# Kernel optimization log

Hardware: AMD Instinct MI355X
Metric: run time of the kernel (lower is better)

## Reference

```python
import jax, jax.numpy as jnp
import numpy as np
from jax import lax

SHIFT = 32  # shift_range from init
EPS_NORM = 1e-12
EPS_MASK = 1e-6


def _l2_normalize_flat(x):
    # F.normalize(x.reshape(B,-1)): per-sample L2 normalize with eps 1e-12
    B = x.shape[0]
    flat = x.reshape(B, -1)
    n = jnp.linalg.norm(flat, axis=1, keepdims=True)
    return (flat / jnp.maximum(n, EPS_NORM)).reshape(x.shape)


def setup_inputs() -> dict:
    key = jax.random.key(0)
    k1, k2 = jax.random.split(key)
    grd_feature = jax.random.normal(k1, (8, 32, 32, 32), dtype=jnp.float32)
    sat_feature = jax.random.normal(k2, (8, 32, 128, 128), dtype=jnp.float32)
    return {"grd_feature": grd_feature, "sat_feature": sat_feature, "test_method": 1}


def reference(grd_feature, sat_feature, test_method):
    # test_method == 1 path (default); test_method in {0,1} only differ in divisor
    M, C, H_s, W_s = sat_feature.shape
    N, _, H, W = grd_feature.shape
    kH = min(H, H_s - 2 * SHIFT)
    kW = min(W, W_s - 2 * SHIFT)

    # center-crop ground template to (kH, kW) and L2-normalize per sample
    gh0, gw0 = H // 2 - kH // 2, W // 2 - kW // 2
    grd = grd_feature[:, :, gh0:gh0 + 2 * (kH // 2), gw0:gw0 + 2 * (kW // 2)]
    N_, _, H_k, W_k = grd.shape
    grd = _l2_normalize_flat(grd)

    # center-crop satellite to search region and L2-normalize per sample
    sh0 = H_s // 2 - SHIFT - kH // 2
    sw0 = W_s // 2 - SHIFT - kW // 2
    sat = sat_feature[:, :, sh0:sh0 + 2 * (SHIFT + kH // 2), sw0:sw0 + 2 * (SHIFT + kW // 2)]
    _, _, H_i, W_i = sat.shape
    sat = _l2_normalize_flat(sat)

    # all-pairs cross-correlation: corr[m, n, y, x] (torch grouped-conv on repeated sat
    # is equivalent to a plain VALID conv of sat with all N ground filters)
    corr = lax.conv_general_dilated(
        sat, grd, window_strides=(1, 1), padding='VALID',
        dimension_numbers=('NCHW', 'OIHW', 'NCHW'))  # [M, N, Ho, Wo]
    Ho, Wo = corr.shape[2], corr.shape[3]

    # sliding-window sum of |sat|^2 (avg_pool with divisor_override=1, summed over C)
    s2 = jnp.sum(sat * sat, axis=1)  # [M, H_i, W_i]
    partical = lax.reduce_window(s2, jnp.float32(0), lax.add,
                                 (1, H_k, W_k), (1, 1, 1), 'VALID')  # [M, Ho, Wo]
    if test_method == 0:
        denom = jnp.sqrt(partical)
    else:
        denom = partical
    corr = corr / jnp.maximum(denom[:, None], EPS_NORM)

    similarity_matrix = jnp.max(corr, axis=(2, 3))  # [M, N]

    # diagonal pairs (m == n): peak localization
    diag = jnp.diagonal(corr, axis1=0, axis2=1)        # [Ho, Wo, M]
    diag = jnp.transpose(diag, (2, 0, 1)).reshape(M, -1)
    max_index = jnp.argmax(diag, axis=-1)
    pos_h = max_index // Wo
    pos_w = max_index % Wo

    grd_mask = (jnp.abs(jnp.sum(grd, axis=1)) > EPS_MASK).astype(jnp.float32)  # [N, H_k, W_k]

    def place(ph, pw, gm):
        z = jnp.zeros((1, H_i, W_i), dtype=jnp.float32)
        return lax.dynamic_update_slice(z, gm[None], (0, ph, pw))

    mask = jax.vmap(place)(pos_h, pos_w, grd_mask)  # [M, 1, H_i, W_i]
    return similarity_matrix, mask
```

## Files before the change

kernel.cpp:

```cpp
#include <hip/hip_runtime.h>
#include <stdint.h>

typedef unsigned short u16;
typedef unsigned int u32;
typedef unsigned long long u64;
typedef __bf16 bf16x8 __attribute__((ext_vector_type(8)));
typedef float floatx4 __attribute__((ext_vector_type(4)));

#define DEVI static __device__ __forceinline__

DEVI u16 f2bf(float f) {
  uint32_t u = __builtin_bit_cast(uint32_t, f);
  u += 0x7FFFu + ((u >> 16) & 1u);
  return (u16)(u >> 16);
}
DEVI float bf2f(u16 b) { return __builtin_bit_cast(float, (uint32_t)b << 16); }

DEVI u32 encf(float f) {
  u32 u = __builtin_bit_cast(u32, f);
  return (u >> 31) ? ~u : (u | 0x80000000u);
}
DEVI float decf(u32 e) {
  u32 u = (e >> 31) ? (e & 0x7FFFFFFFu) : ~e;
  return __builtin_bit_cast(float, u);
}

DEVI void cp16(const u16* g, u16* l) {
#if __has_builtin(__builtin_amdgcn_global_load_lds)
  __builtin_amdgcn_global_load_lds(
      (const __attribute__((address_space(1))) uint32_t*)g,
      (__attribute__((address_space(3))) uint32_t*)l, 16, 0, 0);
#else
  *(uint4*)l = *(const uint4*)g;
#endif
}

static constexpr size_t OFF_CORRP = 0;
static constexpr size_t OFF_SATT  = OFF_CORRP + (size_t)4*270400*4;
static constexpr size_t OFF_GRDP  = OFF_SATT + (size_t)8*4*96*96*8*2;
static constexpr size_t OFF_S2    = OFF_GRDP + (size_t)4*1024*16*8*2;
static constexpr size_t OFF_PART  = OFF_S2   + (size_t)73728*4;
static constexpr size_t OFF_NRMP  = OFF_PART + (size_t)33800*4;
static constexpr size_t OFF_GNRM  = OFF_NRMP + 768*4;
static constexpr size_t OFF_MASK  = OFF_GNRM + 32;
static constexpr size_t OFF_PMAX  = OFF_MASK + (size_t)8192*4;
static constexpr size_t OFF_CNT   = OFF_PMAX + 320*4;
static constexpr size_t OFF_CAND  = OFF_CNT  + 512;

__global__ __launch_bounds__(256) void k_prep(
    const float* __restrict__ grd, const float* __restrict__ sat,
    u16* __restrict__ sTh, u16* __restrict__ gP,
    float* __restrict__ s2, float* __restrict__ nrmp,
    float* __restrict__ gnrm, float* __restrict__ gmask,
    u32* __restrict__ cnts) {
  __shared__ float L[32*100];
  __shared__ float red[256];
  const int t = threadIdx.x;
  if (blockIdx.x < 768) {
    const int m = blockIdx.x / 96, y = blockIdx.x - (blockIdx.x / 96) * 96;
    #pragma unroll
    for (int k = 0; k < 3; ++k) {
      const int idx = k*256 + t;
      const int c = idx / 24, xq = idx - c*24;
      const float4 v = *(const float4*)(sat + (((size_t)m*32 + c)*128 + (16+y))*128 + 16 + xq*4);
      *(float4*)(&L[c*100 + xq*4]) = v;
    }
    __syncthreads();
    float ss = 0.f;
    if (t < 96) {
      #pragma unroll
      for (int c = 0; c < 32; ++c) { const float v = L[c*100 + t]; ss += v*v; }
      s2[(size_t)m*9216 + y*96 + t] = ss;
    }
    red[t] = ss; __syncthreads();
    for (int s = 128; s > 0; s >>= 1) { if (t < s) red[t] += red[t+s]; __syncthreads(); }
    if (t == 0) nrmp[m*96 + y] = red[0];
    for (int idx = t; idx < 384; idx += 256) {
      const int cb = idx / 96, x = idx - cb*96;
      union { u16 us[8]; uint4 v4; } P;
      #pragma unroll
      for (int e = 0; e < 8; ++e) P.us[e] = f2bf(L[(cb*8+e)*100 + x]);
      *(uint4*)(&sTh[(((size_t)m*4+cb)*9216 + (size_t)y*96 + x)*8]) = P.v4;
    }
  } else if (blockIdx.x == 776) {
    if (t < 72) cnts[t] = 0u;
  } else {
    const int n = blockIdx.x - 768;
    float nn = 0.f, scs[4];
    #pragma unroll
    for (int it = 0; it < 4; ++it) {
      const int pidx = it*256 + t;
      float vals[32]; float sc = 0.f;
      #pragma unroll
      for (int c = 0; c < 32; ++c) {
        const float v = grd[((size_t)n*32 + c)*1024 + pidx];
        vals[c] = v; sc += v; nn += v*v;
      }
      scs[it] = sc;
      #pragma unroll
      for (int cb = 0; cb < 4; ++cb) {
        union { u16 us[8]; uint4 v4; } ph, pl;
        #pragma unroll
        for (int e = 0; e < 8; ++e) {
          const float v = vals[cb*8+e];
          const u16 h = f2bf(v); ph.us[e] = h; pl.us[e] = f2bf(v - bf2f(h));
        }
        const size_t o = ((size_t)cb*1024 + pidx)*128;
        *(uint4*)(&gP[o + (size_t)n*8])     = ph.v4;
        *(uint4*)(&gP[o + (size_t)(n+8)*8]) = pl.v4;
      }
    }
    red[t] = nn; __syncthreads();
    for (int s = 128; s > 0; s >>= 1) { if (t < s) red[t] += red[t+s]; __syncthreads(); }
    const float gn = fmaxf(sqrtf(red[0]), 1e-12f);
    if (t == 0) gnrm[n] = red[0];
    const float thr = 1e-6f * gn;
    #pragma unroll
    for (int it = 0; it < 4; ++it)
      gmask[n*1024 + it*256 + t] = (fabsf(scs[it]) > thr) ? 1.f : 0.f;
  }
}

__global__ __launch_bounds__(256, 3) void k_conv(
    const u16* __restrict__ satT, const u16* __restrict__ gP,
    const float* __restrict__ s2, float* __restrict__ corr_p,
    float* __restrict__ part)
{
  __shared__ __align__(16) u16 patch[41*48*8];

  const int bi = blockIdx.x;
  const int tid = threadIdx.x;

  if (bi < 72) {
    float* S  = (float*)patch;
    float* HS = S + 40*96;
    const int pm = bi / 9, ysl = (bi - pm*9)*8;
    const int nrows = (65 - ysl) < 8 ? (65 - ysl) : 8;
    const int scnt  = (96 - ysl) < 40 ? (96 - ysl) : 40;
    for (int idx = tid; idx < scnt*96; idx += 256)
      S[idx] = s2[(size_t)pm*9216 + (size_t)ysl*96 + idx];
    __syncthreads();
    const int hrows = nrows + 31;
    for (int idx = tid; idx < hrows*65; idx += 256) {
      const int r = idx / 65, xo = idx - r*65;
      const float* p = &S[r*96 + xo];
      float s = 0.f;
      #pragma unroll
      for (int j = 0; j < 32; ++j) s += p[j];
      HS[idx] = s;
    }
    __syncthreads();
    for (int idx = tid; idx < nrows*65; idx += 256) {
      const int r = idx / 65, xo = idx - r*65;
      float s = 0.f;
      #pragma unroll
      for (int i = 0; i < 32; ++i) s += HS[(r+i)*65 + xo];
      part[(size_t)pm*4225 + (size_t)(ysl+r)*65 + xo] = s;
    }
    return;
  }

  const int wave = tid >> 6, lane = tid & 63;
  const int pr = lane & 15, q = lane >> 4;

  if (bi >= 968) {
    const int e = bi - 968;
    const int cb = e & 3;
    const int yt = (e >> 2) % 5;
    const int m  = e / 20;
    const int ybase = yt * 13;
    const size_t rowbase = ((size_t)(m*4 + cb) * 96 + ybase) * 96;
    for (int k = tid; k < 44*32; k += 256) {
      const int rho = k >> 5, px = k & 31;
      cp16(&satT[(rowbase + (size_t)rho*96 + 64 + px)*8], &patch[(size_t)k*8]);
    }
    asm volatile("s_waitcnt vmcnt(0)" ::: "memory");
    __syncthreads();
    const int prc = pr < 13 ? pr : 12;
    floatx4 acc = (floatx4){0.f, 0.f, 0.f, 0.f};
    #pragma unroll
    for (int jbi = 0; jbi < 2; ++jbi) {
      const int jb = wave*2 + jbi;
      const int px_e = jb*4 + q;
      const u16* bp = gP + ((size_t)cb*1024 + (size_t)(jb*4+q))*128 + (size_t)pr*8;
      uint4 Br[8];
      #pragma unroll
      for (int ii = 0; ii < 8; ++ii) Br[ii] = *(const uint4*)(bp + (size_t)ii*4096);
      uint4 Ah[8];
      #pragma unroll
      for (int s = 0; s < 6; ++s)
        Ah[s] = *(const uint4*)(&patch[((size_t)(prc + s)*32 + px_e)*8]);
      #pragma unroll
      for (int i = 0; i < 32; ++i) {
        if (i < 26)
          Ah[(i+6)&7] = *(const uint4*)(&patch[((size_t)(prc + i + 6)*32 + px_e)*8]);
        const bf16x8 bf = __builtin_bit_cast(bf16x8, Br[i&7]);
        if (i < 24)
          Br[(i+8)&7] = *(const uint4*)(bp + (size_t)(i+8)*4096);
        acc = __builtin_amdgcn_mfma_f32_16x16x32_bf16(
            __builtin_bit_cast(bf16x8, Ah[i&7]), bf, acc, 0, 0, 0);
      }
    }
    float v4[4];
    #pragma unroll
    for (int k = 0; k < 4; ++k) v4[k] = acc[k] + __shfl_xor(acc[k], 8);
    __syncthreads();
    float* red = (float*)patch;
    #pragma unroll
    for (int k = 0; k < 4; ++k) red[((size_t)wave*64 + lane)*5 + k] = v4[k];
    __syncthreads();
    if (wave == 0 && pr < 8) {
      #pragma unroll
      for (int k = 0; k < 4; ++k) {
        const int yoff = q*4 + k;
        if (yoff < 13) {
          float s = 0.f;
          #pragma unroll
          for (int w = 0; w < 4; ++w) s += red[((size_t)w*64 + lane)*5 + k];
          corr_p[(size_t)cb*270400 + ((size_t)(m*8+pr)*65 + (ybase+yoff))*65 + 64] = s;
        }
      }
    }
    return;
  }

  int b = bi - 72;
  const int cb = b & 3; b >>= 2;
  const int xt = b & 3; b >>= 2;
  const int yt = b % 7;
  const int m  = b / 7;
  const int x0 = xt*16;

  if (yt < 6) {
    const int y0 = yt*10;
    const size_t rowbase = ((size_t)(m*4 + cb) * 96 + y0) * 96;
    for (int k = tid; k < 41*48; k += 256) {
      const int rho = k / 48, px = k - (k/48)*48;
      cp16(&satT[(rowbase + (size_t)rho*96 + x0 + px)*8], &patch[(size_t)k*8]);
    }
    asm volatile("s_waitcnt vmcnt(0)" ::: "memory");
    __syncthreads();

    floatx4 acc[10];
    #pragma unroll
    for (int r = 0; r < 10; ++r) acc[r] = (floatx4){0.f, 0.f, 0.f, 0.f};

    #pragma unroll
    for (int jbi = 0; jbi < 2; ++jbi) {
      const int jb = wave*2 + jbi;
      const int apx = pr + jb*4 + q;
      const u16* bp = gP + ((size_t)cb*1024 + (size_t)(jb*4+q))*128 + (size_t)pr*8;

      uint4 Br[8];
      #pragma unroll
      for (int ii = 0; ii < 8; ++ii) Br[ii] = *(const uint4*)(bp + (size_t)ii*4096);
      uint4 Ah[12];
      #pragma unroll
      for (int s = 0; s < 12; ++s) Ah[s] = *(const uint4*)(&patch[((size_t)s*48 + apx)*8]);

      #pragma unroll
      for (int i = 0; i < 32; ++i) {
        const bf16x8 bf = __builtin_bit_cast(bf16x8, Br[i&7]);
        if (i < 24)
          Br[(i+8)&7] = *(const uint4*)(bp + (size_t)(i+8)*4096);
        #pragma unroll
        for (int r = 0; r < 10; ++r)
          acc[r] = __builtin_amdgcn_mfma_f32_16x16x32_bf16(
              __builtin_bit_cast(bf16x8, Ah[(i+r)%12]), bf, acc[r], 0, 0, 0);
        if (i < 29)
          Ah[(i+12)%12] = *(const uint4*)(&patch[((size_t)(i+12)*48 + apx)*8]);
      }
    }

    float vals[40];
    #pragma unroll
    for (int r = 0; r < 10; ++r)
      #pragma unroll
      for (int k = 0; k < 4; ++k)
        vals[r*4+k] = acc[r][k] + __shfl_xor(acc[r][k], 8);

    float* red = (float*)patch;
    #pragma unroll
    for (int half = 0; half < 2; ++half) {
      __syncthreads();
      #pragma unroll
      for (int u = 0; u < 20; ++u) red[((size_t)wave*64 + lane)*21 + u] = vals[half*20 + u];
      __syncthreads();
      if (wave == 0 && pr < 8) {
        #pragma unroll
        for (int r = 0; r < 5; ++r) {
          #pragma unroll
          for (int k = 0; k < 4; ++k) {
            const int x = x0 + q*4 + k;
            float s = 0.f;
            #pragma unroll
            for (int w = 0; w < 4; ++w) s += red[((size_t)w*64 + lane)*21 + r*4 + k];
            corr_p[(size_t)cb*270400 + ((size_t)(m*8+pr)*65 + (y0 + half*5 + r))*65 + x] = s;
          }
        }
      }
    }
  } else {
    const int y0 = 60;
    const size_t rowbase = ((size_t)(m*4 + cb) * 96 + y0) * 96;
    for (int k = tid; k < 36*48; k += 256) {
      const int rho = k / 48, px = k - (k/48)*48;
      cp16(&satT[(rowbase + (size_t)rho*96 + x0 + px)*8], &patch[(size_t)k*8]);
    }
    asm volatile("s_waitcnt vmcnt(0)" ::: "memory");
    __syncthreads();

    floatx4 acc[5];
    #pragma unroll
    for (int r = 0; r < 5; ++r) acc[r] = (floatx4){0.f, 0.f, 0.f, 0.f};

    #pragma unroll
    for (int jbi = 0; jbi < 2; ++jbi) {
      const int jb = wave*2 + jbi;
      const int apx = pr + jb*4 + q;
      const u16* bp = gP + ((size_t)cb*1024 + (size_t)(jb*4+q))*128 + (size_t)pr*8;

      uint4 Br[8];
      #pragma unroll
      for (int ii = 0; ii < 8; ++ii) Br[ii] = *(const uint4*)(bp + (size_t)ii*4096);
      uint4 Ah[8];
      #pragma unroll
      for (int s = 0; s < 6; ++s) Ah[s] = *(const uint4*)(&patch[((size_t)s*48 + apx)*8]);

      #pragma unroll
      for (int i = 0; i < 32; ++i) {
        if (i < 30)
          Ah[(i+6)&7] = *(const uint4*)(&patch[((size_t)(i+6)*48 + apx)*8]);
        const bf16x8 bf = __builtin_bit_cast(bf16x8, Br[i&7]);
        if (i < 24)
          Br[(i+8)&7] = *(const uint4*)(bp + (size_t)(i+8)*4096);
        #pragma unroll
        for (int r = 0; r < 5; ++r)
          acc[r] = __builtin_amdgcn_mfma_f32_16x16x32_bf16(
              __builtin_bit_cast(bf16x8, Ah[(i+r)&7]), bf, acc[r], 0, 0, 0);
      }
    }

    float vals[20];
    #pragma unroll
    for (int r = 0; r < 5; ++r)
      #pragma unroll
      for (int k = 0; k < 4; ++k)
        vals[r*4+k] = acc[r][k] + __shfl_xor(acc[r][k], 8);

    __syncthreads();
    float* red = (float*)patch;
    #pragma unroll
    for (int u = 0; u < 20; ++u) red[((size_t)wave*64 + lane)*21 + u] = vals[u];
    __syncthreads();
    if (wave == 0 && pr < 8) {
      #pragma unroll
      for (int r = 0; r < 5; ++r) {
        #pragma unroll
        for (int k = 0; k < 4; ++k) {
          const int x = x0 + q*4 + k;
          float s = 0.f;
          #pragma unroll
          for (int w = 0; w < 4; ++w) s += red[((size_t)w*64 + lane)*21 + r*4 + k];
          corr_p[(size_t)cb*270400 + ((size_t)(m*8+pr)*65 + (y0+r))*65 + x] = s;
        }
      }
    }
  }
}

__global__ __launch_bounds__(256) void k_post(
    const float* __restrict__ corr_p, const float* __restrict__ part,
    const float* __restrict__ nrmp, const float* __restrict__ gnrm,
    const int* __restrict__ tm, const float* __restrict__ grd,
    const float* __restrict__ sat, const float* __restrict__ gmask,
    u32* __restrict__ pmaxE, u32* __restrict__ grpcnt,
    u32* __restrict__ candcnt, u64* __restrict__ cand,
    float* __restrict__ out)
{
  __shared__ float red[256];
  __shared__ float s_bcast;
  __shared__ int s_last;
  __shared__ int fidx[128];
  __shared__ u32 fcnt;

  const int bi = blockIdx.x;
  const int m = bi / 40, n = (bi / 5) & 7, yc = bi % 5, g = m*8 + n;
  const int t = threadIdx.x;
  const bool diag = (m == n);

  red[t] = (t < 96) ? nrmp[m*96 + t] : 0.f;
  __syncthreads();
  for (int s = 128; s > 0; s >>= 1) { if (t < s) red[t] += red[t+s]; __syncthreads(); }
  const float srn = 1.f / fmaxf(sqrtf(red[0]), 1e-12f);
  const float grn = 1.f / fmaxf(sqrtf(gnrm[n]), 1e-12f);
  const float cscale = grn * srn, pscale = srn * srn;
  const int method = tm[0];

  const float* cp = corr_p + (size_t)g*4225;
  const float* pp = part + (size_t)m*4225;
  const int i0 = yc*845, i1 = i0 + 845;
  float vv[4];
  float bestv = -3.4e38f;
  #pragma unroll
  for (int k = 0; k < 4; ++k) {
    const int idx = i0 + k*256 + t;
    float v = -3.4e38f;
    if (idx < i1) {
      const float c = cp[idx] + cp[idx+270400] + cp[idx+540800] + cp[idx+811200];
      const float pt = pp[idx] * pscale;
      float denom = (method == 0) ? sqrtf(pt) : pt;
      denom = fmaxf(denom, 1e-12f);
      v = c * cscale / denom;
    }
    vv[k] = v;
    bestv = fmaxf(bestv, v);
  }
  __syncthreads();
  red[t] = bestv; __syncthreads();
  for (int s = 128; s > 0; s >>= 1) { if (t < s) red[t] = fmaxf(red[t], red[t+s]); __syncthreads(); }
  if (t == 0) { s_bcast = red[0]; atomicExch(&pmaxE[bi], encf(red[0])); }
  __syncthreads();
  if (diag) {
    const float lthr = s_bcast - 3e-3f;
    #pragma unroll
    for (int k = 0; k < 4; ++k) {
      const int idx = i0 + k*256 + t;
      if (idx < i1 && vv[k] >= lthr) {
        const u32 s = atomicAdd(&candcnt[n], 1u);
        if (s < 128)
          atomicExch(&cand[n*128 + s],
                     ((u64)__builtin_bit_cast(u32, vv[k]) << 32) | (u32)idx);
      }
    }
  }
  __syncthreads();
  if (t == 0) s_last = (atomicAdd(&grpcnt[g], 1u) == 4u) ? 1 : 0;
  __syncthreads();
  if (!s_last) return;

  if (t == 0) {
    float gm = -3.4e38f;
    #pragma unroll
    for (int k = 0; k < 5; ++k) gm = fmaxf(gm, decf(atomicOr(&pmaxE[g*5 + k], 0u)));
    out[g] = gm;
    s_bcast = gm;
  }
  __syncthreads();
  if (!diag) return;

  const float gmax = s_bcast;
  const float thr = gmax - 3e-3f;
  if (t == 0) fcnt = 0u;
  __syncthreads();
  u32 nc = atomicAdd(&candcnt[n], 0u); if (nc > 128) nc = 128;
  if (t < (int)nc) {
    const u64 pk = atomicAdd(&cand[n*128 + t], 0ULL);
    const float vf = __builtin_bit_cast(float, (u32)(pk >> 32));
    const int idx = (int)(u32)pk;
    if (vf >= thr) { const u32 s = atomicAdd(&fcnt, 1u); fidx[s] = idx; }
  }
  __syncthreads();
  if (t == 0 && fcnt == 0u) { fidx[0] = 0; fcnt = 1u; }
  __syncthreads();
  const int nf = (int)fcnt;

  __shared__ float sbest; __shared__ int sbix;
  if (t == 0) { sbest = -3.4e38f; sbix = 0x7FFFFFFF; }
  __syncthreads();
  const int c = t >> 3, s8 = t & 7;
  for (int ci = 0; ci < nf; ++ci) {
    const int idx = fidx[ci];
    const int y = idx / 65, x = idx - y*65;
    float a = 0.f;
    #pragma unroll
    for (int ii = 0; ii < 4; ++ii) {
      const int i = s8 + ii*8;
      const float* gr = grd + ((size_t)n*32 + c)*1024 + i*32;
      const float* sr = sat + (((size_t)n*32 + c)*128 + (16 + y + i))*128 + (16 + x);
      #pragma unroll
      for (int j = 0; j < 32; ++j) a += gr[j] * sr[j];
    }
    red[t] = a; __syncthreads();
    for (int st = 128; st > 0; st >>= 1) { if (t < st) red[t] += red[t+st]; __syncthreads(); }
    if (t == 0) {
      const float pt = part[(size_t)n*4225 + idx] * pscale;
      float denom = (method == 0) ? sqrtf(pt) : pt;
      denom = fmaxf(denom, 1e-12f);
      const float v = red[0] * cscale / denom;
      if (v > sbest || (v == sbest && idx < sbix)) { sbest = v; sbix = idx; }
    }
    __syncthreads();
  }
  const int bix = sbix;
  const int ph = bix / 65, pw = bix - (bix/65)*65;
  for (int p = t; p < 9216; p += 256) {
    const int yy = p / 96, xx = p - yy*96;
    float val = 0.f;
    if (yy >= ph && yy < ph+32 && xx >= pw && xx < pw+32)
      val = gmask[n*1024 + (yy-ph)*32 + (xx-pw)];
    out[64 + (size_t)n*9216 + p] = val;
  }
}

extern "C" void kernel_launch(void* const* d_in, const int* in_sizes, int n_in,
                              void* d_out, int out_size, void* d_ws, size_t ws_size,
                              hipStream_t stream) {
  const float* grd = (const float*)d_in[0];
  const float* sat = (const float*)d_in[1];
  const int*   tm  = (const int*)d_in[2];
  float* out = (float*)d_out;
  char* ws = (char*)d_ws;

  float* corrp = (float*)(ws + OFF_CORRP);
  u16*   sTh   = (u16*)(ws + OFF_SATT);
  u16*   gP    = (u16*)(ws + OFF_GRDP);
  float* s2    = (float*)(ws + OFF_S2);
  float* part  = (float*)(ws + OFF_PART);
  float* nrmp  = (float*)(ws + OFF_NRMP);
  float* gnrm  = (float*)(ws + OFF_GNRM);
  float* gmask = (float*)(ws + OFF_MASK);
  u32*   pmaxE = (u32*)(ws + OFF_PMAX);
  u32*   cnts  = (u32*)(ws + OFF_CNT);
  u64*   cand  = (u64*)(ws + OFF_CAND);

  k_prep<<<777,  256, 0, stream>>>(grd, sat, sTh, gP, s2, nrmp, gnrm, gmask, cnts);
  k_conv<<<1128, 256, 0, stream>>>(sTh, gP, s2, corrp, part);
  k_post<<<320,  256, 0, stream>>>(corrp, part, nrmp, gnrm, tm, grd, sat, gmask,
                                   pmaxE, cnts, cnts + 64, cand, out);
}
```

Before: 149.1 us.

## Use wave-shuffle reductions, MFMA priority hints, and split conv epilogue across waves

After: 145.6 us. -2.4%, faster.

```diff
diff --git a/kernel.cpp b/kernel.cpp
--- a/kernel.cpp
+++ b/kernel.cpp
@@ -23,6 +23,17 @@
 DEVI float decf(u32 e) {
   u32 u = (e >> 31) ? (e & 0x7FFFFFFFu) : ~e;
   return __builtin_bit_cast(float, u);
+}
+
+DEVI float wred_sum(float v) {
+  #pragma unroll
+  for (int o = 32; o > 0; o >>= 1) v += __shfl_xor(v, o);
+  return v;
+}
+DEVI float wred_max(float v) {
+  #pragma unroll
+  for (int o = 32; o > 0; o >>= 1) v = fmaxf(v, __shfl_xor(v, o));
+  return v;
 }
 
 DEVI void cp16(const u16* g, u16* l) {
@@ -54,7 +65,7 @@
     float* __restrict__ gnrm, float* __restrict__ gmask,
     u32* __restrict__ cnts) {
   __shared__ float L[32*100];
-  __shared__ float red[256];
+  __shared__ float red[4];
   const int t = threadIdx.x;
   if (blockIdx.x < 768) {
     const int m = blockIdx.x / 96, y = blockIdx.x - (blockIdx.x / 96) * 96;
@@ -72,9 +83,10 @@
       for (int c = 0; c < 32; ++c) { const float v = L[c*100 + t]; ss += v*v; }
       s2[(size_t)m*9216 + y*96 + t] = ss;
     }
-    red[t] = ss; __syncthreads();
-    for (int s = 128; s > 0; s >>= 1) { if (t < s) red[t] += red[t+s]; __syncthreads(); }
-    if (t == 0) nrmp[m*96 + y] = red[0];
+    const float wsum = wred_sum(ss);
+    if ((t & 63) == 0) red[t >> 6] = wsum;
+    __syncthreads();
+    if (t == 0) nrmp[m*96 + y] = red[0] + red[1] + red[2] + red[3];
     for (int idx = t; idx < 384; idx += 256) {
       const int cb = idx / 96, x = idx - cb*96;
       union { u16 us[8]; uint4 v4; } P;
@@ -110,10 +122,12 @@
         *(uint4*)(&gP[o + (size_t)(n+8)*8]) = pl.v4;
       }
     }
-    red[t] = nn; __syncthreads();
-    for (int s = 128; s > 0; s >>= 1) { if (t < s) red[t] += red[t+s]; __syncthreads(); }
-    const float gn = fmaxf(sqrtf(red[0]), 1e-12f);
-    if (t == 0) gnrm[n] = red[0];
+    const float tot = wred_sum(nn);
+    if ((t & 63) == 0) red[t >> 6] = tot;
+    __syncthreads();
+    const float sum = red[0] + red[1] + red[2] + red[3];
+    if (t == 0) gnrm[n] = sum;
+    const float gn = fmaxf(sqrtf(sum), 1e-12f);
     const float thr = 1e-6f * gn;
     #pragma unroll
     for (int it = 0; it < 4; ++it)
@@ -263,40 +277,36 @@
         const bf16x8 bf = __builtin_bit_cast(bf16x8, Br[i&7]);
         if (i < 24)
           Br[(i+8)&7] = *(const uint4*)(bp + (size_t)(i+8)*4096);
+        __builtin_amdgcn_s_setprio(1);
         #pragma unroll
         for (int r = 0; r < 10; ++r)
           acc[r] = __builtin_amdgcn_mfma_f32_16x16x32_bf16(
               __builtin_bit_cast(bf16x8, Ah[(i+r)%12]), bf, acc[r], 0, 0, 0);
+        __builtin_amdgcn_s_setprio(0);
         if (i < 29)
           Ah[(i+12)%12] = *(const uint4*)(&patch[((size_t)(i+12)*48 + apx)*8]);
       }
     }
 
-    float vals[40];
-    #pragma unroll
-    for (int r = 0; r < 10; ++r)
-      #pragma unroll
-      for (int k = 0; k < 4; ++k)
-        vals[r*4+k] = acc[r][k] + __shfl_xor(acc[r][k], 8);
-
     float* red = (float*)patch;
     #pragma unroll
     for (int half = 0; half < 2; ++half) {
       __syncthreads();
       #pragma unroll
-      for (int u = 0; u < 20; ++u) red[((size_t)wave*64 + lane)*21 + u] = vals[half*20 + u];
+      for (int u = 0; u < 20; ++u)
+        red[((size_t)wave*64 + lane)*21 + u] = acc[half*5 + (u>>2)][u&3];
       __syncthreads();
-      if (wave == 0 && pr < 8) {
+      if (pr < 8) {
+        const int fw = wave;
         #pragma unroll
         for (int r = 0; r < 5; ++r) {
+          float s = 0.f;
           #pragma unroll
-          for (int k = 0; k < 4; ++k) {
-            const int x = x0 + q*4 + k;
-            float s = 0.f;
-            #pragma unroll
-            for (int w = 0; w < 4; ++w) s += red[((size_t)w*64 + lane)*21 + r*4 + k];
-            corr_p[(size_t)cb*270400 + ((size_t)(m*8+pr)*65 + (y0 + half*5 + r))*65 + x] = s;
-          }
+          for (int w = 0; w < 4; ++w)
+            s += red[((size_t)w*64 + lane)*21 + r*4 + fw]
+               + red[((size_t)w*64 + (lane^8))*21 + r*4 + fw];
+          const int x = x0 + q*4 + fw;
+          corr_p[(size_t)cb*270400 + ((size_t)(m*8+pr)*65 + (y0 + half*5 + r))*65 + x] = s;
         }
       }
     }
@@ -334,36 +344,32 @@
         const bf16x8 bf = __builtin_bit_cast(bf16x8, Br[i&7]);
         if (i < 24)
           Br[(i+8)&7] = *(const uint4*)(bp + (size_t)(i+8)*4096);
+        __builtin_amdgcn_s_setprio(1);
         #pragma unroll
         for (int r = 0; r < 5; ++r)
           acc[r] = __builtin_amdgcn_mfma_f32_16x16x32_bf16(
               __builtin_bit_cast(bf16x8, Ah[(i+r)&7]), bf, acc[r], 0, 0, 0);
-      }
-    }
-
-    float vals[20];
-    #pragma unroll
-    for (int r = 0; r < 5; ++r)
-      #pragma unroll
-      for (int k = 0; k < 4; ++k)
-        vals[r*4+k] = acc[r][k] + __shfl_xor(acc[r][k], 8);
+        __builtin_amdgcn_s_setprio(0);
+      }
+    }
 
     __syncthreads();
     float* red = (float*)patch;
     #pragma unroll
-    for (int u = 0; u < 20; ++u) red[((size_t)wave*64 + lane)*21 + u] = vals[u];
-    __syncthreads();
-    if (wave == 0 && pr < 8) {
+    for (int u = 0; u < 20; ++u)
+      red[((size_t)wave*64 + lane)*21 + u] = acc[u>>2][u&3];
+    __syncthreads();
+    if (pr < 8) {
+      const int fw = wave;
       #pragma unroll
       for (int r = 0; r < 5; ++r) {
+        float s = 0.f;
         #pragma unroll
-        for (int k = 0; k < 4; ++k) {
-          const int x = x0 + q*4 + k;
-          float s = 0.f;
-          #pragma unroll
-          for (int w = 0; w < 4; ++w) s += red[((size_t)w*64 + lane)*21 + r*4 + k];
-          corr_p[(size_t)cb*270400 + ((size_t)(m*8+pr)*65 + (y0+r))*65 + x] = s;
-        }
+        for (int w = 0; w < 4; ++w)
+          s += red[((size_t)w*64 + lane)*21 + r*4 + fw]
+             + red[((size_t)w*64 + (lane^8))*21 + r*4 + fw];
+        const int x = x0 + q*4 + fw;
+        corr_p[(size_t)cb*270400 + ((size_t)(m*8+pr)*65 + (y0+r))*65 + x] = s;
       }
     }
   }
@@ -378,8 +384,7 @@
     u32* __restrict__ candcnt, u64* __restrict__ cand,
     float* __restrict__ out)
 {
-  __shared__ float red[256];
-  __shared__ float s_bcast;
+  __shared__ float red[8];
   __shared__ int s_last;
   __shared__ int fidx[128];
   __shared__ u32 fcnt;
@@ -387,12 +392,15 @@
   const int bi = blockIdx.x;
   const int m = bi / 40, n = (bi / 5) & 7, yc = bi % 5, g = m*8 + n;
   const int t = threadIdx.x;
+  const int wv = t >> 6, ln = t & 63;
   const bool diag = (m == n);
 
-  red[t] = (t < 96) ? nrmp[m*96 + t] : 0.f;
-  __syncthreads();
-  for (int s = 128; s > 0; s >>= 1) { if (t < s) red[t] += red[t+s]; __syncthreads(); }
-  const float srn = 1.f / fmaxf(sqrtf(red[0]), 1e-12f);
+  float v0 = (t < 96) ? nrmp[m*96 + t] : 0.f;
+  v0 = wred_sum(v0);
+  if (ln == 0) red[wv] = v0;
+  __syncthreads();
+  const float snrm2 = red[0] + red[1] + red[2] + red[3];
+  const float srn = 1.f / fmaxf(sqrtf(snrm2), 1e-12f);
   const float grn = 1.f / fmaxf(sqrtf(gnrm[n]), 1e-12f);
   const float cscale = grn * srn, pscale = srn * srn;
   const int method = tm[0];
@@ -417,12 +425,13 @@
     bestv = fmaxf(bestv, v);
   }
   __syncthreads();
-  red[t] = bestv; __syncthreads();
-  for (int s = 128; s > 0; s >>= 1) { if (t < s) red[t] = fmaxf(red[t], red[t+s]); __syncthreads(); }
-  if (t == 0) { s_bcast = red[0]; atomicExch(&pmaxE[bi], encf(red[0])); }
-  __syncthreads();
+  const float bw = wred_max(bestv);
+  if (ln == 0) red[wv] = bw;
+  __syncthreads();
+  const float bmax = fmaxf(fmaxf(red[0], red[1]), fmaxf(red[2], red[3]));
+  if (t == 0) atomicExch(&pmaxE[bi], encf(bmax));
   if (diag) {
-    const float lthr = s_bcast - 3e-3f;
+    const float lthr = bmax - 3e-3f;
     #pragma unroll
     for (int k = 0; k < 4; ++k) {
       const int idx = i0 + k*256 + t;
@@ -439,17 +448,12 @@
   __syncthreads();
   if (!s_last) return;
 
-  if (t == 0) {
-    float gm = -3.4e38f;
-    #pragma unroll
-    for (int k = 0; k < 5; ++k) gm = fmaxf(gm, decf(atomicOr(&pmaxE[g*5 + k], 0u)));
-    out[g] = gm;
-    s_bcast = gm;
-  }
-  __syncthreads();
+  if (t < 5) red[t] = decf(atomicOr(&pmaxE[g*5 + t], 0u));
+  __syncthreads();
+  const float gmax = fmaxf(fmaxf(fmaxf(red[0], red[1]), fmaxf(red[2], red[3])), red[4]);
+  if (t == 0) out[g] = gmax;
   if (!diag) return;
 
-  const float gmax = s_bcast;
   const float thr = gmax - 3e-3f;
   if (t == 0) fcnt = 0u;
   __syncthreads();
@@ -481,13 +485,15 @@
       #pragma unroll
       for (int j = 0; j < 32; ++j) a += gr[j] * sr[j];
     }
-    red[t] = a; __syncthreads();
-    for (int st = 128; st > 0; st >>= 1) { if (t < st) red[t] += red[t+st]; __syncthreads(); }
+    a = wred_sum(a);
+    if (ln == 0) red[wv] = a;
+    __syncthreads();
     if (t == 0) {
+      const float tot = red[0] + red[1] + red[2] + red[3];
       const float pt = part[(size_t)n*4225 + idx] * pscale;
       float denom = (method == 0) ? sqrtf(pt) : pt;
       denom = fmaxf(denom, 1e-12f);
-      const float v = red[0] * cscale / denom;
+      const float v = tot * cscale / denom;
       if (v > sbest || (v == sbest && idx < sbix)) { sbest = v; sbix = idx; }
     }
     __syncthreads();
```
